# Optimization experiments

Hardware: AMD Instinct MI355X
Metric: run time of the kernel (lower is better)

The kernel has to match this reference:

```python
import jax, jax.numpy as jnp
import numpy as np

C = 64; H = 80; W = 120; B = 2; V = 3; BV = B * V; D = 20
NEAR = 0.1; FAR = 100.0
BF16 = jnp.bfloat16


def conv2d(x, w, b, pad):
    y = jax.lax.conv_general_dilated(x, w, (1, 1), [(pad, pad), (pad, pad)],
                                     dimension_numbers=('NCHW', 'OIHW', 'NCHW'))
    return y + b[None, :, None, None]


def bn2d(x, g, b, m, v, eps=1e-5):
    # BatchNorm2d in inference mode (running stats)
    scale = g / jnp.sqrt(v + eps)
    return (x - m[None, :, None, None]) * scale[None, :, None, None] + b[None, :, None, None]


def grid_sample(feat, grid):
    # feat [N,C,Hf,Wf], grid [N,Hg,Wg,2] in [-1,1]; bilinear, zeros padding, align_corners=True
    _, _, Hf, Wf = feat.shape
    gx = (grid[..., 0] + 1.0) * 0.5 * (Wf - 1)
    gy = (grid[..., 1] + 1.0) * 0.5 * (Hf - 1)
    x0 = jnp.floor(gx); y0 = jnp.floor(gy)

    def one(f, gx, gy, x0, y0):
        def gather(xi, yi):
            valid = (xi >= 0) & (xi < Wf) & (yi >= 0) & (yi < Hf)
            xc = jnp.clip(xi, 0, Wf - 1).astype(jnp.int32)
            yc = jnp.clip(yi, 0, Hf - 1).astype(jnp.int32)
            return f[:, yc, xc] * valid.astype(f.dtype)
        wx = gx - x0; wy = gy - y0
        return (gather(x0, y0) * ((1 - wx) * (1 - wy))
                + gather(x0 + 1, y0) * (wx * (1 - wy))
                + gather(x0, y0 + 1) * ((1 - wx) * wy)
                + gather(x0 + 1, y0 + 1) * (wx * wy))
    return jax.vmap(one)(feat, gx, gy, x0, y0)


def forward(x, intrinsics, c2ws,
            pf_bn1_g, pf_bn1_b, pf_bn1_m, pf_bn1_v, pf_w1, pf_b1,
            pf_bn2_g, pf_bn2_b, pf_bn2_m, pf_bn2_v, pf_w2, pf_b2,
            cp_w, cp_b, cf_bn_g, cf_bn_b, cf_bn_m, cf_bn_v, cf_w, cf_b):
    # ---- flag[0]: predicted depth -> world xyz, position_fusion ----
    depth = 255.0 * (0.5 * jnp.tanh(x[:, 0]) + 0.5)                       # [BV,H,W]
    d16 = depth.astype(BF16)
    ug = jnp.broadcast_to(jnp.arange(W, dtype=jnp.float32)[None, :], (H, W)).astype(BF16)
    vg = jnp.broadcast_to(jnp.arange(H, dtype=jnp.float32)[:, None], (H, W)).astype(BF16)
    cam = jnp.stack([ug[None] * d16, vg[None] * d16, d16], axis=-1).reshape(BV, H * W, 3)
    Kinv = jnp.linalg.inv(intrinsics.astype(jnp.float32)).astype(BF16)
    xyz = jnp.einsum('nij,npj->npi', Kinv, cam)                           # cam coords
    xyz = jnp.einsum('nij,npj->npi', c2ws[:, :3, :3].astype(BF16), xyz) \
          + c2ws[:, :3, 3].astype(BF16)[:, None, :]                       # world coords
    xyz = xyz.reshape(BV, H, W, 3).transpose(0, 3, 1, 2).astype(x.dtype)
    h = jnp.concatenate([xyz, x], axis=1)                                 # [BV,C+3,H,W]
    h = jax.nn.silu(conv2d(bn2d(h, pf_bn1_g, pf_bn1_b, pf_bn1_m, pf_bn1_v), pf_w1, pf_b1, 4))
    h = jax.nn.silu(conv2d(bn2d(h, pf_bn2_g, pf_bn2_b, pf_bn2_m, pf_bn2_v), pf_w2, pf_b2, 4))

    # ---- flag[1]: multi-view plane-sweep correlation ----
    xr = h.reshape(B, V, C, H, W)
    vb = lambda t: t.transpose(1, 0, 2, 3, 4).reshape(BV, C, H, W)        # 'b v ... -> (v b) ...'
    feat01 = vb(xr)
    Ki = intrinsics.reshape(B, V, 3, 3)
    intr_curr = jax.lax.stop_gradient(
        (Ki * jnp.array([W, H, 1.0], jnp.float32)[None, None, :, None]).transpose(1, 0, 2, 3).reshape(BV, 3, 3))
    E = jax.lax.stop_gradient(c2ws.reshape(B, V, 4, 4))
    Einv = jnp.linalg.inv(E)
    dmin, dmax = 1.0 / FAR, 1.0 / NEAR
    depth_vals = 1.0 / (dmin + jnp.linspace(0.0, 1.0, D) * (dmax - dmin))  # [D]
    pix = jnp.stack([jnp.broadcast_to(jnp.arange(W, dtype=jnp.float32)[None, :], (H, W)),
                     jnp.broadcast_to(jnp.arange(H, dtype=jnp.float32)[:, None], (H, W)),
                     jnp.ones((H, W), jnp.float32)], 0).reshape(3, H * W)
    Kinv_c = jnp.linalg.inv(intr_curr).astype(BF16)

    corr = 0.0
    for idx in range(1, V):
        order = list(range(V))[idx:] + list(range(V))[:idx]
        feat10 = vb(xr[:, jnp.array(order)])                              # [BV,C,H,W]
        pose = jnp.concatenate([E[:, o] @ Einv[:, v0] for v0, o in enumerate(order)], axis=0)  # [BV,4,4]
        pts = jnp.einsum('bij,jp->bip', Kinv_c, pix.astype(BF16))
        pts = jnp.einsum('bij,bjp->bip', pose[:, :3, :3].astype(BF16), pts)
        pts = pts[:, :, None, :] * depth_vals.astype(BF16)[None, None, :, None] \
              + pose[:, :3, 3].astype(BF16)[:, :, None, None]             # [BV,3,D,HW]
        pts = jnp.einsum('bij,bjdp->bidp', intr_curr.astype(BF16), pts).astype(jnp.float32)
        den = jnp.maximum(pts[:, 2], 1e-3)
        grid = jnp.stack([2.0 * pts[:, 0] / den / (W - 1) - 1.0,
                          2.0 * pts[:, 1] / den / (H - 1) - 1.0], axis=-1)
        grid = jax.lax.stop_gradient(grid.reshape(BV, D * H, W, 2))
        warped = grid_sample(feat10, grid).reshape(BV, C, D, H, W)
        corr = corr + jnp.einsum('bchw,bcdhw->bdhw', feat01, warped) / (C ** 0.5)
    corr = corr / (V - 1)

    cin = jnp.concatenate([corr, feat01], axis=1)                         # [BV,D+C,H,W]
    cost = conv2d(cin, cp_w, cp_b, 1).reshape(V, B, C, H, W).transpose(1, 0, 2, 3, 4)
    fused = jnp.concatenate([cost, xr], axis=2).reshape(BV, 2 * C, H, W)
    out = jax.nn.silu(conv2d(bn2d(fused, cf_bn_g, cf_bn_b, cf_bn_m, cf_bn_v), cf_w, cf_b, 4))
    return out


def setup_inputs() -> dict:
    key = jax.random.key(0)
    ks = jax.random.split(key, 24)
    def nrm(i, shape, scale=1.0):
        return scale * jax.random.normal(ks[i], shape, jnp.float32)
    def wconv(i, shape):
        fan_in = int(np.prod(shape[1:]))
        return jax.random.normal(ks[i], shape, jnp.float32) / np.sqrt(fan_in)
    x = nrm(0, (BV, C, H, W))
    Kmat = np.tile(np.array([[1.2, 0, 0.5], [0, 1.6, 0.5], [0, 0, 1.0]], np.float32), (BV, 1, 1))
    intrinsics = jnp.asarray(Kmat)
    c2_list = []
    for i in range(BV):
        th = 0.3 * (i % V) - 0.3
        T = np.eye(4, dtype=np.float32)
        T[:3, :3] = np.array([[np.cos(th), 0, np.sin(th)], [0, 1, 0], [-np.sin(th), 0, np.cos(th)]], np.float32)
        T[:3, 3] = [0.5 * (i % V) - 0.5, 0.0, 0.1]
        c2_list.append(T)
    c2ws = jnp.asarray(np.stack(c2_list))
    # first BN sees raw world-xyz channels (magnitude ~1e4), so realistic running var there
    bn1_v = jnp.concatenate([jnp.full((3,), 1e8, jnp.float32), jnp.ones((C,), jnp.float32)])
    return dict(
        x=x, intrinsics=intrinsics, c2ws=c2ws,
        pf_bn1_g=1.0 + 0.1 * nrm(1, (C + 3,)), pf_bn1_b=0.1 * nrm(2, (C + 3,)),
        pf_bn1_m=0.1 * nrm(3, (C + 3,)), pf_bn1_v=bn1_v,
        pf_w1=wconv(4, (C, C + 3, 9, 9)), pf_b1=0.01 * nrm(5, (C,)),
        pf_bn2_g=1.0 + 0.1 * nrm(6, (C,)), pf_bn2_b=0.1 * nrm(7, (C,)),
        pf_bn2_m=0.1 * nrm(8, (C,)), pf_bn2_v=jnp.ones((C,), jnp.float32),
        pf_w2=wconv(9, (C, C, 9, 9)), pf_b2=0.01 * nrm(10, (C,)),
        cp_w=wconv(11, (C, C + D, 3, 3)), cp_b=0.01 * nrm(12, (C,)),
        cf_bn_g=1.0 + 0.1 * nrm(13, (2 * C,)), cf_bn_b=0.1 * nrm(14, (2 * C,)),
        cf_bn_m=0.1 * nrm(15, (2 * C,)), cf_bn_v=jnp.ones((2 * C,), jnp.float32),
        cf_w=wconv(16, (C, 2 * C, 9, 9)), cf_b=0.01 * nrm(17, (C,)))


def reference(x, intrinsics, c2ws,
              pf_bn1_g, pf_bn1_b, pf_bn1_m, pf_bn1_v, pf_w1, pf_b1,
              pf_bn2_g, pf_bn2_b, pf_bn2_m, pf_bn2_v, pf_w2, pf_b2,
              cp_w, cp_b, cf_bn_g, cf_bn_b, cf_bn_m, cf_bn_v, cf_w, cf_b):
    return forward(x, intrinsics, c2ws,
                   pf_bn1_g, pf_bn1_b, pf_bn1_m, pf_bn1_v, pf_w1, pf_b1,
                   pf_bn2_g, pf_bn2_b, pf_bn2_m, pf_bn2_v, pf_w2, pf_b2,
                   cp_w, cp_b, cf_bn_g, cf_bn_b, cf_bn_m, cf_bn_v, cf_w, cf_b)
```

## Files before the change

### kernel.cpp

```cpp
#include <hip/hip_runtime.h>
#include <math.h>

static constexpr int kH  = 80;
static constexpr int kW  = 120;
static constexpr int kHW = kH * kW;
static constexpr int kBV = 6;
static constexpr int kD  = 20;

typedef __attribute__((ext_vector_type(8)))  short bf16x8;
typedef __attribute__((ext_vector_type(16))) float f32x16;
typedef __attribute__((ext_vector_type(4)))  int   i32x4;
typedef __attribute__((ext_vector_type(2)))  int   i32x2;
typedef __attribute__((ext_vector_type(4)))  float float4v;

__device__ __forceinline__ float bf16r(float x) {
  unsigned u = __float_as_uint(x);
  u += 0x7FFFu + ((u >> 16) & 1u);
  return __uint_as_float(u & 0xFFFF0000u);
}
__device__ __forceinline__ unsigned short bf16c(float x) {
  unsigned u = __float_as_uint(x);
  u += 0x7FFFu + ((u >> 16) & 1u);
  return (unsigned short)(u >> 16);
}
__device__ __forceinline__ int pack2(float a, float b) {
  return (int)((unsigned)bf16c(a) | ((unsigned)bf16c(b) << 16));
}

struct ConstBuf {
  float bn1_s[67], bn1_o[67];
  float bn2_s[64], bn2_o[64];
  float bnf_s[128], bnf_o[128];
  float Kinv[6][9];
  float Rw[6][9];
  float tw[6][3];
  float Kinvc[6][9];
  float intrc[6][9];
  float poseR[2][6][9];
  float poseT[2][6][3];
  float dvals[20];
};

__device__ void inv3x3(const float* A, float* o) {
  float a = A[0], b = A[1], c = A[2];
  float d = A[3], e = A[4], f = A[5];
  float g = A[6], h = A[7], i = A[8];
  float det = a * (e * i - f * h) - b * (d * i - f * g) + c * (d * h - e * g);
  float id = 1.0f / det;
  o[0] = (e * i - f * h) * id;
  o[1] = -(b * i - c * h) * id;
  o[2] = (b * f - c * e) * id;
  o[3] = -(d * i - f * g) * id;
  o[4] = (a * i - c * g) * id;
  o[5] = -(a * f - c * d) * id;
  o[6] = (d * h - e * g) * id;
  o[7] = -(a * h - b * g) * id;
  o[8] = (a * e - b * d) * id;
}

__device__ void inv4x4(const float* A, float* out) {
  float M[4][8];
  for (int r = 0; r < 4; ++r) {
    for (int c = 0; c < 4; ++c) M[r][c] = A[r * 4 + c];
    for (int c = 0; c < 4; ++c) M[r][4 + c] = (r == c) ? 1.0f : 0.0f;
  }
  for (int col = 0; col < 4; ++col) {
    int p = col;
    float best = fabsf(M[col][col]);
    for (int r = col + 1; r < 4; ++r) {
      float v = fabsf(M[r][col]);
      if (v > best) { best = v; p = r; }
    }
    if (p != col)
      for (int c = 0; c < 8; ++c) { float t = M[col][c]; M[col][c] = M[p][c]; M[p][c] = t; }
    float inv = 1.0f / M[col][col];
    for (int c = 0; c < 8; ++c) M[col][c] *= inv;
    for (int r = 0; r < 4; ++r) {
      if (r == col) continue;
      float f = M[r][col];
      for (int c = 0; c < 8; ++c) M[r][c] -= f * M[col][c];
    }
  }
  for (int r = 0; r < 4; ++r)
    for (int c = 0; c < 4; ++c) out[r * 4 + c] = M[r][4 + c];
}

__device__ void mm4(const float* A, const float* B, float* C) {
  for (int r = 0; r < 4; ++r)
    for (int c = 0; c < 4; ++c) {
      float s = 0.0f;
      for (int k = 0; k < 4; ++k) s += A[r * 4 + k] * B[k * 4 + c];
      C[r * 4 + c] = s;
    }
}

__global__ void consts_kernel(const float* __restrict__ intr, const float* __restrict__ c2,
                              const float* g1, const float* b1, const float* m1, const float* v1,
                              const float* g2, const float* b2, const float* m2, const float* v2,
                              const float* gf, const float* bff, const float* mf, const float* vff,
                              ConstBuf* cb) {
  int tid = threadIdx.x;
  for (int c = tid; c < 67; c += 64) {
    float s = g1[c] / sqrtf(v1[c] + 1e-5f);
    cb->bn1_s[c] = s; cb->bn1_o[c] = b1[c] - m1[c] * s;
  }
  for (int c = tid; c < 64; c += 64) {
    float s = g2[c] / sqrtf(v2[c] + 1e-5f);
    cb->bn2_s[c] = s; cb->bn2_o[c] = b2[c] - m2[c] * s;
  }
  for (int c = tid; c < 128; c += 64) {
    float s = gf[c] / sqrtf(vff[c] + 1e-5f);
    cb->bnf_s[c] = s; cb->bnf_o[c] = bff[c] - mf[c] * s;
  }
  if (tid < 20) {
    float l = (1.0f / 19.0f) * (float)tid;
    cb->dvals[tid] = bf16r(1.0f / (0.01f + l * 9.99f));
  }
  __shared__ float Einv_s[6][16];
  if (tid < 6) {
    float Ki[9];
    inv3x3(intr + tid * 9, Ki);
    for (int k = 0; k < 9; ++k) cb->Kinv[tid][k] = bf16r(Ki[k]);
    const float* T = c2 + tid * 16;
    cb->Rw[tid][0] = bf16r(T[0]);  cb->Rw[tid][1] = bf16r(T[1]);  cb->Rw[tid][2] = bf16r(T[2]);
    cb->Rw[tid][3] = bf16r(T[4]);  cb->Rw[tid][4] = bf16r(T[5]);  cb->Rw[tid][5] = bf16r(T[6]);
    cb->Rw[tid][6] = bf16r(T[8]);  cb->Rw[tid][7] = bf16r(T[9]);  cb->Rw[tid][8] = bf16r(T[10]);
    cb->tw[tid][0] = bf16r(T[3]);  cb->tw[tid][1] = bf16r(T[7]);  cb->tw[tid][2] = bf16r(T[11]);
    inv4x4(T, Einv_s[tid]);
    int vj = tid >> 1, bj = tid & 1, ii = bj * 3 + vj;
    const float* Kk = intr + ii * 9;
    float S[9] = {Kk[0] * 120.0f, Kk[1] * 120.0f, Kk[2] * 120.0f,
                  Kk[3] * 80.0f,  Kk[4] * 80.0f,  Kk[5] * 80.0f,
                  Kk[6],          Kk[7],          Kk[8]};
    for (int k = 0; k < 9; ++k) cb->intrc[tid][k] = bf16r(S[k]);
    float Si[9];
    inv3x3(S, Si);
    for (int k = 0; k < 9; ++k) cb->Kinvc[tid][k] = bf16r(Si[k]);
  }
  __syncthreads();
  if (tid < 12) {
    int t = tid / 6, jj = tid % 6;
    int vj = jj >> 1, bj = jj & 1;
    int o = (vj + t + 1) % 3;
    float P[16];
    mm4(c2 + (bj * 3 + o) * 16, Einv_s[bj * 3 + vj], P);
    for (int r = 0; r < 3; ++r) {
      for (int c = 0; c < 3; ++c) cb->poseR[t][jj][r * 3 + c] = bf16r(P[r * 4 + c]);
      cb->poseT[t][jj][r] = bf16r(P[r * 4 + 3]);
    }
  }
}

template <int K, int CINP, int CINR>
__global__ __launch_bounds__(256)
void prep_w(const float* __restrict__ w, unsigned short* __restrict__ Wp) {
  constexpr int NCH = CINP / 32;
  constexpr int NU = K * K * NCH * 256;
  int u = blockIdx.x * 256 + threadIdx.x;
  if (u >= NU) return;
  int slot = u & 255;
  int rest = u >> 8;
  int ci = rest % NCH;
  int kk = rest / NCH;
  int ky = kk / K, kx = kk - ky * K;
  int oc = slot >> 2;
  int gi = (slot & 3) ^ ((oc >> 2) & 3);
  int chb = ci * 32 + gi * 8;
  unsigned short o[8];
#pragma unroll
  for (int e = 0; e < 8; ++e) {
    int ch = chb + e;
    float val = (ch < CINR) ? w[(((size_t)oc * CINR + ch) * K + ky) * K + kx] : 0.0f;
    o[e] = bf16c(val);
  }
  i32x4 pk;
  pk.x = (int)o[0] | ((int)o[1] << 16);
  pk.y = (int)o[2] | ((int)o[3] << 16);
  pk.z = (int)o[4] | ((int)o[5] << 16);
  pk.w = (int)o[6] | ((int)o[7] << 16);
  *(i32x4*)&Wp[(size_t)u * 8] = pk;
}

__global__ __launch_bounds__(256)
void hn_pack(const float* __restrict__ x, const ConstBuf* __restrict__ cb,
             unsigned short* __restrict__ hn_b) {
  int id = blockIdx.x * 256 + threadIdx.x;
  if (id >= kBV * kHW) return;
  int bv = id / kHW, pix = id - bv * kHW;
  int yy = pix / kW, xx = pix - yy * kW;
  float t0 = tanhf(x[(size_t)bv * 64 * kHW + pix]);
  float depth = 255.0f * (0.5f * t0 + 0.5f);
  float dz = bf16r(depth);
  float cx = bf16r((float)xx * dz);
  float cy = bf16r((float)yy * dz);
  const float* Ki = cb->Kinv[bv];
  float p0 = bf16r(Ki[0] * cx + Ki[1] * cy + Ki[2] * dz);
  float p1 = bf16r(Ki[3] * cx + Ki[4] * cy + Ki[5] * dz);
  float p2 = bf16r(Ki[6] * cx + Ki[7] * cy + Ki[8] * dz);
  const float* R = cb->Rw[bv];
  const float* tw = cb->tw[bv];
  float q[3];
  q[0] = bf16r(bf16r(R[0] * p0 + R[1] * p1 + R[2] * p2) + tw[0]);
  q[1] = bf16r(bf16r(R[3] * p0 + R[4] * p1 + R[5] * p2) + tw[1]);
  q[2] = bf16r(bf16r(R[6] * p0 + R[7] * p1 + R[8] * p2) + tw[2]);
  unsigned short* o = &hn_b[(size_t)id * 96];
  const float* xb = x + (size_t)bv * 64 * kHW + pix;
#pragma unroll
  for (int g = 0; g < 24; ++g) {
    float vv[4];
#pragma unroll
    for (int e = 0; e < 4; ++e) {
      int ch = g * 4 + e;
      float val;
      if (ch < 3) val = q[ch] * cb->bn1_s[ch] + cb->bn1_o[ch];
      else if (ch < 67) val = xb[(size_t)(ch - 3) * kHW] * cb->bn1_s[ch] + cb->bn1_o[ch];
      else val = 0.0f;
      vv[e] = val;
    }
    i32x2 pk = {pack2(vv[0], vv[1]), pack2(vv[2], vv[3])};
    *(i32x2*)(o + g * 4) = pk;
  }
}

template <int CINP, int K, int OUT>
__global__ __launch_bounds__(256)
void conv_mfma(const unsigned short* __restrict__ in_b,
               const unsigned short* __restrict__ Wp,
               const float* __restrict__ bias,
               const ConstBuf* __restrict__ cb,
               float* __restrict__ outf,
               unsigned short* __restrict__ outb) {
  constexpr int NCH = CINP / 32;
  constexpr int KK = K * K;
  constexpr int GN = KK / 3;
  constexpr int PAD = K / 2;
  constexpr int NC = 16 + K - 1;
  constexpr int NR = 8 + K - 1;
  constexpr int NPX = NC * NR;
  __shared__ unsigned short sA[NPX * 32];
  __shared__ unsigned short sB[2][3 * 2048];

  const int tid = threadIdx.x;
  const int w = tid >> 6, l = tid & 63;
  const int bx = blockIdx.x, by = blockIdx.y, bz = blockIdx.z;
  const size_t inbase = (size_t)bz * kHW;

  const int r = l & 31, h = l >> 5;
  const int xloc = r & 15;
  const int ybase = 2 * w + (r >> 4);
  f32x16 acc[2] = {};

  int boff[2][2];
#pragma unroll
  for (int nt = 0; nt < 2; ++nt)
#pragma unroll
    for (int kc = 0; kc < 2; ++kc) {
      int oc = nt * 32 + (l & 31);
      int gi = kc * 2 + h;
      boff[nt][kc] = (oc * 4 + (gi ^ ((oc >> 2) & 3))) * 8;
    }

  for (int ci = 0; ci < NCH; ++ci) {
    for (int g2 = tid; g2 < NPX * 4; g2 += 256) {
      int px = g2 >> 2, gi = g2 & 3;
      int hy = px / NC, hx = px - hy * NC;
      int gy = by * 8 - PAD + hy, gx = bx * 16 - PAD + hx;
      bool ok = ((unsigned)gy < (unsigned)kH) && ((unsigned)gx < (unsigned)kW);
      i32x4 v = {0, 0, 0, 0};
      if (ok) v = *(const i32x4*)&in_b[(inbase + gy * kW + gx) * CINP + ci * 32 + gi * 8];
      *(i32x4*)&sA[px * 32 + ((gi ^ ((px >> 2) & 3)) << 3)] = v;
    }
#pragma unroll
    for (int t = 0; t < 3; ++t) {
      int u = tid + t * 256;
      int kki = u >> 8, slot = u & 255;
      *(i32x4*)&sB[0][u * 8] =
          *(const i32x4*)&Wp[(((size_t)kki * NCH + ci) * 256 + slot) * 8];
    }
    __syncthreads();

    for (int g = 0; g < GN; ++g) {
      const int cur = g & 1, nxt = cur ^ 1;
      const bool hasnext = (g + 1 < GN);
      i32x4 pf[3];
      if (hasnext) {
#pragma unroll
        for (int t = 0; t < 3; ++t) {
          int u = tid + t * 256;
          int kki = u >> 8, slot = u & 255;
          pf[t] = *(const i32x4*)
              &Wp[(((size_t)((g + 1) * 3 + kki) * NCH + ci) * 256 + slot) * 8];
        }
      }
#pragma unroll
      for (int kki = 0; kki < 3; ++kki) {
        const int kk = g * 3 + kki;
        const int ky = kk / K, kx = kk - ky * K;
        const int hp = (ybase + ky) * NC + (xloc + kx);
        bf16x8 a[2];
#pragma unroll
        for (int kc = 0; kc < 2; ++kc) {
          int gi = kc * 2 + h;
          a[kc] = *(const bf16x8*)&sA[hp * 32 + ((gi ^ ((hp >> 2) & 3)) << 3)];
        }
        bf16x8 bb[2][2];
#pragma unroll
        for (int nt = 0; nt < 2; ++nt)
#pragma unroll
          for (int kc = 0; kc < 2; ++kc)
            bb[nt][kc] = *(const bf16x8*)&sB[cur][kki * 2048 + boff[nt][kc]];
#pragma unroll
        for (int nt = 0; nt < 2; ++nt) {
          acc[nt] = __builtin_amdgcn_mfma_f32_32x32x16_bf16(a[0], bb[nt][0], acc[nt], 0, 0, 0);
          acc[nt] = __builtin_amdgcn_mfma_f32_32x32x16_bf16(a[1], bb[nt][1], acc[nt], 0, 0, 0);
        }
      }
      if (hasnext) {
#pragma unroll
        for (int t = 0; t < 3; ++t)
          *(i32x4*)&sB[nxt][(tid + t * 256) * 8] = pf[t];
      }
      __syncthreads();
    }
  }

#pragma unroll
  for (int nt = 0; nt < 2; ++nt) {
    const int oc = nt * 32 + (l & 31);
    const float bs = bias[oc];
    float s2 = 0.f, o2 = 0.f;
    if (OUT == 0) { s2 = cb->bn2_s[oc]; o2 = cb->bn2_o[oc]; }
    if (OUT == 2) { s2 = cb->bnf_s[oc]; o2 = cb->bnf_o[oc]; }
#pragma unroll
    for (int reg = 0; reg < 16; ++reg) {
      int row = (reg & 3) + 8 * (reg >> 2) + 4 * h;
      int x = bx * 16 + (row & 15);
      if (x >= kW) continue;
      int y = by * 8 + 2 * w + (row >> 4);
      float v = acc[nt][reg] + bs;
      if (OUT != 2) v = v / (1.0f + expf(-v));
      if (OUT == 0) {
        size_t px = inbase + y * kW + x;
        outb[px * 64 + oc] = bf16c(v * s2 + o2);
      } else if (OUT == 1) {
        size_t px = inbase + y * kW + x;
        outf[px * 64 + oc] = v;
      } else if (OUT == 2) {
        int i = (bz & 1) * 3 + (bz >> 1);
        size_t px = (size_t)i * kHW + y * kW + x;
        outb[px * 128 + oc] = bf16c(v * s2 + o2);
      } else {
        outf[((size_t)bz * 64 + oc) * kHW + y * kW + x] = v;
      }
    }
  }
}

__global__ __launch_bounds__(256)
void corr_kernel(const float* __restrict__ h, const ConstBuf* __restrict__ cb,
                 unsigned short* __restrict__ cin_b) {
  __shared__ float sgeo[4][40][8];
  const int tid = threadIdx.x;
  const int w = tid >> 6, lane = tid & 63;
  const int wid = blockIdx.x * 4 + w;
  const int j = wid / kHW;
  const int pix = wid - j * kHW;
  const int yy = pix / kW, xx = pix - yy * kW;
  const int b = j & 1, v = j >> 1;
  const float f01 = h[((size_t)(b * 3 + v) * kHW + pix) * 64 + lane];
  const char* sb0 = (const char*)(h + (size_t)(b * 3 + ((v + 1) % 3)) * kHW * 64);
  const char* sb1 = (const char*)(h + (size_t)(b * 3 + ((v + 2) % 3)) * kHW * 64);

  if (lane < 40) {
    const int d = lane >> 1, t = lane & 1;
    const float* Kc = cb->Kinvc[j];
    const float* IC = cb->intrc[j];
    const float uf = (float)xx, vf = (float)yy;
    float p1_0 = bf16r(Kc[0] * uf + Kc[1] * vf + Kc[2]);
    float p1_1 = bf16r(Kc[3] * uf + Kc[4] * vf + Kc[5]);
    float p1_2 = bf16r(Kc[6] * uf + Kc[7] * vf + Kc[8]);
    const float* PR = cb->poseR[t][j];
    const float* PT = cb->poseT[t][j];
    float p20 = bf16r(PR[0] * p1_0 + PR[1] * p1_1 + PR[2] * p1_2);
    float p21 = bf16r(PR[3] * p1_0 + PR[4] * p1_1 + PR[5] * p1_2);
    float p22 = bf16r(PR[6] * p1_0 + PR[7] * p1_1 + PR[8] * p1_2);
    float dv = cb->dvals[d];
    float q0 = bf16r(bf16r(p20 * dv) + PT[0]);
    float q1 = bf16r(bf16r(p21 * dv) + PT[1]);
    float q2 = bf16r(bf16r(p22 * dv) + PT[2]);
    float s0 = bf16r(IC[0] * q0 + IC[1] * q1 + IC[2] * q2);
    float s1 = bf16r(IC[3] * q0 + IC[4] * q1 + IC[5] * q2);
    float s2 = bf16r(IC[6] * q0 + IC[7] * q1 + IC[8] * q2);
    float den = fmaxf(s2, 1e-3f);
    float g0 = 2.0f * s0 / den / 119.0f - 1.0f;
    float g1 = 2.0f * s1 / den / 79.0f - 1.0f;
    float gx = (g0 + 1.0f) * 0.5f * 119.0f;
    float gy = (g1 + 1.0f) * 0.5f * 79.0f;
    float x0f = floorf(gx), y0f = floorf(gy);
    float wx = gx - x0f, wy = gy - y0f;
    float x1f = x0f + 1.0f, y1f = y0f + 1.0f;
    float vx0 = (x0f >= 0.0f && x0f < 120.0f) ? 1.0f : 0.0f;
    float vx1 = (x1f >= 0.0f && x1f < 120.0f) ? 1.0f : 0.0f;
    float vy0 = (y0f >= 0.0f && y0f < 80.0f) ? 1.0f : 0.0f;
    float vy1 = (y1f >= 0.0f && y1f < 80.0f) ? 1.0f : 0.0f;
    int xi0 = (int)fminf(fmaxf(x0f, 0.0f), 119.0f);
    int xi1 = (int)fminf(fmaxf(x1f, 0.0f), 119.0f);
    int yi0 = (int)fminf(fmaxf(y0f, 0.0f), 79.0f);
    int yi1 = (int)fminf(fmaxf(y1f, 0.0f), 79.0f);
    int r0b = yi0 * (kW * 256), r1b = yi1 * (kW * 256);
    int c0b = xi0 * 256, c1b = xi1 * 256;
    float* gp = sgeo[w][lane];
    gp[0] = __int_as_float(r0b + c0b);
    gp[1] = __int_as_float(r0b + c1b);
    gp[2] = __int_as_float(r1b + c0b);
    gp[3] = __int_as_float(r1b + c1b);
    gp[4] = ((1.0f - wx) * (1.0f - wy)) * (vx0 * vy0);
    gp[5] = (wx * (1.0f - wy)) * (vx1 * vy0);
    gp[6] = ((1.0f - wx) * wy) * (vx0 * vy1);
    gp[7] = (wx * wy) * (vx1 * vy1);
  }
  __syncthreads();

  const unsigned lane4 = (unsigned)lane * 4u;
  unsigned short* op = &cin_b[(size_t)wid * 96];
#pragma unroll 2
  for (int d = 0; d < kD; ++d) {
    float a = 0.0f;
#pragma unroll
    for (int t = 0; t < 2; ++t) {
      const char* sb = t ? sb1 : sb0;
      const float* gp = sgeo[w][d * 2 + t];
      float4v ga = *(const float4v*)gp;
      float4v gb = *(const float4v*)(gp + 4);
      float v00 = *(const float*)(sb + ((unsigned)__float_as_int(ga.x) + lane4));
      float v10 = *(const float*)(sb + ((unsigned)__float_as_int(ga.y) + lane4));
      float v01 = *(const float*)(sb + ((unsigned)__float_as_int(ga.z) + lane4));
      float v11 = *(const float*)(sb + ((unsigned)__float_as_int(ga.w) + lane4));
      a += gb.x * v00 + gb.y * v10 + gb.z * v01 + gb.w * v11;
    }
    float r = a * f01;
#pragma unroll
    for (int off = 32; off > 0; off >>= 1) r += __shfl_xor(r, off, 64);
    if (lane == 0) op[d] = bf16c(r * 0.0625f);
  }
}

__global__ __launch_bounds__(256)
void pack_cin(const float* __restrict__ h, unsigned short* __restrict__ cin_b) {
  int id = blockIdx.x * 256 + threadIdx.x;
  if (id >= kBV * kHW) return;
  int j = id / kHW, pix = id - j * kHW;
  int src = (j & 1) * 3 + (j >> 1);
  const float* hr = &h[((size_t)src * kHW + pix) * 64];
  unsigned short* o = &cin_b[(size_t)id * 96];
#pragma unroll
  for (int g = 0; g < 16; ++g) {
    float4v vv = *(const float4v*)(hr + g * 4);
    i32x2 pk = {pack2(vv.x, vv.y), pack2(vv.z, vv.w)};
    *(i32x2*)(o + 20 + g * 4) = pk;
  }
  i32x2 z = {0, 0};
  *(i32x2*)(o + 84) = z;
  *(i32x2*)(o + 88) = z;
  *(i32x2*)(o + 92) = z;
}

__global__ __launch_bounds__(256)
void pack_fusedn(const float* __restrict__ h, const ConstBuf* __restrict__ cb,
                 unsigned short* __restrict__ fusedn_b) {
  int id = blockIdx.x * 256 + threadIdx.x;
  if (id >= kBV * kHW) return;
  const float* hr = &h[(size_t)id * 64];
  unsigned short* o = &fusedn_b[(size_t)id * 128 + 64];
#pragma unroll
  for (int g = 0; g < 16; ++g) {
    float4v vv = *(const float4v*)(hr + g * 4);
    float r0 = vv.x * cb->bnf_s[64 + g * 4 + 0] + cb->bnf_o[64 + g * 4 + 0];
    float r1 = vv.y * cb->bnf_s[64 + g * 4 + 1] + cb->bnf_o[64 + g * 4 + 1];
    float r2 = vv.z * cb->bnf_s[64 + g * 4 + 2] + cb->bnf_o[64 + g * 4 + 2];
    float r3 = vv.w * cb->bnf_s[64 + g * 4 + 3] + cb->bnf_o[64 + g * 4 + 3];
    i32x2 pk = {pack2(r0, r1), pack2(r2, r3)};
    *(i32x2*)(o + g * 4) = pk;
  }
}

extern "C" void kernel_launch(void* const* d_in, const int* in_sizes, int n_in,
                              void* d_out, int out_size, void* d_ws, size_t ws_size,
                              hipStream_t stream) {
  (void)in_sizes; (void)n_in; (void)out_size; (void)ws_size;
  const float* x    = (const float*)d_in[0];
  const float* intr = (const float*)d_in[1];
  const float* c2w  = (const float*)d_in[2];
  const float* bn1g = (const float*)d_in[3];
  const float* bn1b = (const float*)d_in[4];
  const float* bn1m = (const float*)d_in[5];
  const float* bn1v = (const float*)d_in[6];
  const float* w1   = (const float*)d_in[7];
  const float* b1   = (const float*)d_in[8];
  const float* bn2g = (const float*)d_in[9];
  const float* bn2b = (const float*)d_in[10];
  const float* bn2m = (const float*)d_in[11];
  const float* bn2v = (const float*)d_in[12];
  const float* w2   = (const float*)d_in[13];
  const float* b2   = (const float*)d_in[14];
  const float* cpw  = (const float*)d_in[15];
  const float* cpb  = (const float*)d_in[16];
  const float* bnfg = (const float*)d_in[17];
  const float* bnfb = (const float*)d_in[18];
  const float* bnfm = (const float*)d_in[19];
  const float* bnfv = (const float*)d_in[20];
  const float* wf   = (const float*)d_in[21];
  const float* bff  = (const float*)d_in[22];

  char* ws = (char*)d_ws;
  ConstBuf* cb            = (ConstBuf*)ws;
  unsigned short* hn_b    = (unsigned short*)(ws + 8192);
  unsigned short* h1_b    = (unsigned short*)(ws + 11067392);
  float*          h       = (float*)(ws + 18440192);
  unsigned short* cin_b   = (unsigned short*)(ws + 33185792);
  unsigned short* fused_b = (unsigned short*)(ws + 44244992);
  unsigned short* Wp1     = (unsigned short*)(ws + 58990592);
  unsigned short* Wp2     = (unsigned short*)(ws + 59985920);
  unsigned short* Wpc     = (unsigned short*)(ws + 60649472);
  unsigned short* Wpf     = (unsigned short*)(ws + 60760064);

  consts_kernel<<<1, 64, 0, stream>>>(intr, c2w, bn1g, bn1b, bn1m, bn1v,
                                      bn2g, bn2b, bn2m, bn2v, bnfg, bnfb, bnfm, bnfv, cb);
  prep_w<9, 96, 67><<<243, 256, 0, stream>>>(w1, Wp1);
  prep_w<9, 64, 64><<<162, 256, 0, stream>>>(w2, Wp2);
  prep_w<3, 96, 84><<<27, 256, 0, stream>>>(cpw, Wpc);
  prep_w<9, 128, 128><<<324, 256, 0, stream>>>(wf, Wpf);
  hn_pack<<<225, 256, 0, stream>>>(x, cb, hn_b);

  dim3 cgrid(8, 10, 6);
  conv_mfma<96, 9, 0><<<cgrid, 256, 0, stream>>>(hn_b, Wp1, b1, cb, nullptr, h1_b);
  conv_mfma<64, 9, 1><<<cgrid, 256, 0, stream>>>(h1_b, Wp2, b2, cb, h, nullptr);
  corr_kernel<<<14400, 256, 0, stream>>>(h, cb, cin_b);
  pack_cin<<<225, 256, 0, stream>>>(h, cin_b);
  conv_mfma<96, 3, 2><<<cgrid, 256, 0, stream>>>(cin_b, Wpc, cpb, cb, nullptr, fused_b);
  pack_fusedn<<<225, 256, 0, stream>>>(h, cb, fused_b);
  conv_mfma<128, 9, 3><<<cgrid, 256, 0, stream>>>(fused_b, Wpf, bff, cb, (float*)d_out, nullptr);
}
```

Baseline: 403.0 us.

## Store conv2 output as bf16, fuse pack kernels into conv2 epilogue and corr

Conv2 now writes its output as bf16 and also writes the BN-normalized half of the fusion input directly, which removes the pack_fusedn kernel. The correlation kernel reads bf16 features with each wave handling two pixels (32 lanes each, two channels per lane). It also writes the feature copy and zero padding into cin, which removes pack_cin. The goal is to halve gather traffic and drop two launches. The cost is rounding the correlation features to bf16 earlier than before, which may change numerics slightly.

```diff
diff --git a/kernel.cpp b/kernel.cpp
--- a/kernel.cpp
+++ b/kernel.cpp
@@ -25,6 +25,12 @@
 }
 __device__ __forceinline__ int pack2(float a, float b) {
   return (int)((unsigned)bf16c(a) | ((unsigned)bf16c(b) << 16));
+}
+__device__ __forceinline__ float bl(unsigned pk) {
+  return __uint_as_float(pk << 16);
+}
+__device__ __forceinline__ float bh(unsigned pk) {
+  return __uint_as_float(pk & 0xFFFF0000u);
 }
 
 struct ConstBuf {
@@ -229,7 +235,8 @@
                const float* __restrict__ bias,
                const ConstBuf* __restrict__ cb,
                float* __restrict__ outf,
-               unsigned short* __restrict__ outb) {
+               unsigned short* __restrict__ outb,
+               unsigned short* __restrict__ outb2) {
   constexpr int NCH = CINP / 32;
   constexpr int KK = K * K;
   constexpr int GN = KK / 3;
@@ -330,6 +337,7 @@
     const float bs = bias[oc];
     float s2 = 0.f, o2 = 0.f;
     if (OUT == 0) { s2 = cb->bn2_s[oc]; o2 = cb->bn2_o[oc]; }
+    if (OUT == 1) { s2 = cb->bnf_s[64 + oc]; o2 = cb->bnf_o[64 + oc]; }
     if (OUT == 2) { s2 = cb->bnf_s[oc]; o2 = cb->bnf_o[oc]; }
 #pragma unroll
     for (int reg = 0; reg < 16; ++reg) {
@@ -344,7 +352,8 @@
         outb[px * 64 + oc] = bf16c(v * s2 + o2);
       } else if (OUT == 1) {
         size_t px = inbase + y * kW + x;
-        outf[px * 64 + oc] = v;
+        outb[px * 64 + oc] = bf16c(v);
+        outb2[px * 128 + 64 + oc] = bf16c(v * s2 + o2);
       } else if (OUT == 2) {
         int i = (bz & 1) * 3 + (bz >> 1);
         size_t px = (size_t)i * kHW + y * kW + x;
@@ -357,25 +366,32 @@
 }
 
 __global__ __launch_bounds__(256)
-void corr_kernel(const float* __restrict__ h, const ConstBuf* __restrict__ cb,
+void corr_kernel(const unsigned short* __restrict__ h_b, const ConstBuf* __restrict__ cb,
                  unsigned short* __restrict__ cin_b) {
-  __shared__ float sgeo[4][40][8];
+  __shared__ float sgeo[4][2][40][8];
   const int tid = threadIdx.x;
   const int w = tid >> 6, lane = tid & 63;
-  const int wid = blockIdx.x * 4 + w;
-  const int j = wid / kHW;
-  const int pix = wid - j * kHW;
-  const int yy = pix / kW, xx = pix - yy * kW;
+  const int pair = blockIdx.x * 4 + w;
+  const int j = pair / (kHW / 2);
+  const int pix = (pair - j * (kHW / 2)) * 2;
   const int b = j & 1, v = j >> 1;
-  const float f01 = h[((size_t)(b * 3 + v) * kHW + pix) * 64 + lane];
-  const char* sb0 = (const char*)(h + (size_t)(b * 3 + ((v + 1) % 3)) * kHW * 64);
-  const char* sb1 = (const char*)(h + (size_t)(b * 3 + ((v + 2) % 3)) * kHW * 64);
-
-  if (lane < 40) {
-    const int d = lane >> 1, t = lane & 1;
+  const int ph = lane >> 5, cl = lane & 31;
+  const int pixl = pix + ph;
+  const int dst = b * 3 + v;
+  const unsigned f01pk =
+      ((const unsigned*)(h_b + ((size_t)dst * kHW + pixl) * 64))[cl];
+  const float f01lo = bl(f01pk), f01hi = bh(f01pk);
+  const char* sb0 = (const char*)(h_b + (size_t)(b * 3 + ((v + 1) % 3)) * kHW * 64);
+  const char* sb1 = (const char*)(h_b + (size_t)(b * 3 + ((v + 2) % 3)) * kHW * 64);
+
+  for (int job = lane; job < 80; job += 64) {
+    const int p = job / 40, jj = job - p * 40;
+    const int d = jj >> 1, t = jj & 1;
+    const int pp = pix + p;
+    const int yyp = pp / kW, xxp = pp - yyp * kW;
     const float* Kc = cb->Kinvc[j];
     const float* IC = cb->intrc[j];
-    const float uf = (float)xx, vf = (float)yy;
+    const float uf = (float)xxp, vf = (float)yyp;
     float p1_0 = bf16r(Kc[0] * uf + Kc[1] * vf + Kc[2]);
     float p1_1 = bf16r(Kc[3] * uf + Kc[4] * vf + Kc[5]);
     float p1_2 = bf16r(Kc[6] * uf + Kc[7] * vf + Kc[8]);
@@ -407,9 +423,9 @@
     int xi1 = (int)fminf(fmaxf(x1f, 0.0f), 119.0f);
     int yi0 = (int)fminf(fmaxf(y0f, 0.0f), 79.0f);
     int yi1 = (int)fminf(fmaxf(y1f, 0.0f), 79.0f);
-    int r0b = yi0 * (kW * 256), r1b = yi1 * (kW * 256);
-    int c0b = xi0 * 256, c1b = xi1 * 256;
-    float* gp = sgeo[w][lane];
+    int r0b = yi0 * (kW * 128), r1b = yi1 * (kW * 128);
+    int c0b = xi0 * 128, c1b = xi1 * 128;
+    float* gp = sgeo[w][p][jj];
     gp[0] = __int_as_float(r0b + c0b);
     gp[1] = __int_as_float(r0b + c1b);
     gp[2] = __int_as_float(r1b + c0b);
@@ -421,66 +437,31 @@
   }
   __syncthreads();
 
-  const unsigned lane4 = (unsigned)lane * 4u;
-  unsigned short* op = &cin_b[(size_t)wid * 96];
+  unsigned short* op = &cin_b[(size_t)(j * kHW + pixl) * 96];
+  *(unsigned*)(op + 20 + 2 * cl) = f01pk;
+  if (cl < 6) *(unsigned*)(op + 84 + 2 * cl) = 0u;
+
+  const unsigned cl4 = (unsigned)cl * 4u;
 #pragma unroll 2
   for (int d = 0; d < kD; ++d) {
     float a = 0.0f;
 #pragma unroll
     for (int t = 0; t < 2; ++t) {
       const char* sb = t ? sb1 : sb0;
-      const float* gp = sgeo[w][d * 2 + t];
+      const float* gp = sgeo[w][ph][d * 2 + t];
       float4v ga = *(const float4v*)gp;
       float4v gb = *(const float4v*)(gp + 4);
-      float v00 = *(const float*)(sb + ((unsigned)__float_as_int(ga.x) + lane4));
-      float v10 = *(const float*)(sb + ((unsigned)__float_as_int(ga.y) + lane4));
-      float v01 = *(const float*)(sb + ((unsigned)__float_as_int(ga.z) + lane4));
-      float v11 = *(const float*)(sb + ((unsigned)__float_as_int(ga.w) + lane4));
-      a += gb.x * v00 + gb.y * v10 + gb.z * v01 + gb.w * v11;
-    }
-    float r = a * f01;
-#pragma unroll
-    for (int off = 32; off > 0; off >>= 1) r += __shfl_xor(r, off, 64);
-    if (lane == 0) op[d] = bf16c(r * 0.0625f);
-  }
-}
-
-__global__ __launch_bounds__(256)
-void pack_cin(const float* __restrict__ h, unsigned short* __restrict__ cin_b) {
-  int id = blockIdx.x * 256 + threadIdx.x;
-  if (id >= kBV * kHW) return;
-  int j = id / kHW, pix = id - j * kHW;
-  int src = (j & 1) * 3 + (j >> 1);
-  const float* hr = &h[((size_t)src * kHW + pix) * 64];
-  unsigned short* o = &cin_b[(size_t)id * 96];
-#pragma unroll
-  for (int g = 0; g < 16; ++g) {
-    float4v vv = *(const float4v*)(hr + g * 4);
-    i32x2 pk = {pack2(vv.x, vv.y), pack2(vv.z, vv.w)};
-    *(i32x2*)(o + 20 + g * 4) = pk;
-  }
-  i32x2 z = {0, 0};
-  *(i32x2*)(o + 84) = z;
-  *(i32x2*)(o + 88) = z;
-  *(i32x2*)(o + 92) = z;
-}
-
-__global__ __launch_bounds__(256)
-void pack_fusedn(const float* __restrict__ h, const ConstBuf* __restrict__ cb,
-                 unsigned short* __restrict__ fusedn_b) {
-  int id = blockIdx.x * 256 + threadIdx.x;
-  if (id >= kBV * kHW) return;
-  const float* hr = &h[(size_t)id * 64];
-  unsigned short* o = &fusedn_b[(size_t)id * 128 + 64];
-#pragma unroll
-  for (int g = 0; g < 16; ++g) {
-    float4v vv = *(const float4v*)(hr + g * 4);
-    float r0 = vv.x * cb->bnf_s[64 + g * 4 + 0] + cb->bnf_o[64 + g * 4 + 0];
-    float r1 = vv.y * cb->bnf_s[64 + g * 4 + 1] + cb->bnf_o[64 + g * 4 + 1];
-    float r2 = vv.z * cb->bnf_s[64 + g * 4 + 2] + cb->bnf_o[64 + g * 4 + 2];
-    float r3 = vv.w * cb->bnf_s[64 + g * 4 + 3] + cb->bnf_o[64 + g * 4 + 3];
-    i32x2 pk = {pack2(r0, r1), pack2(r2, r3)};
-    *(i32x2*)(o + g * 4) = pk;
+      unsigned k00 = *(const unsigned*)(sb + ((unsigned)__float_as_int(ga.x) + cl4));
+      unsigned k10 = *(const unsigned*)(sb + ((unsigned)__float_as_int(ga.y) + cl4));
+      unsigned k01 = *(const unsigned*)(sb + ((unsigned)__float_as_int(ga.z) + cl4));
+      unsigned k11 = *(const unsigned*)(sb + ((unsigned)__float_as_int(ga.w) + cl4));
+      float al = gb.x * bl(k00) + gb.y * bl(k10) + gb.z * bl(k01) + gb.w * bl(k11);
+      float ah = gb.x * bh(k00) + gb.y * bh(k10) + gb.z * bh(k01) + gb.w * bh(k11);
+      a += al * f01lo + ah * f01hi;
+    }
+#pragma unroll
+    for (int off = 16; off > 0; off >>= 1) a += __shfl_xor(a, off, 64);
+    if (cl == 0) op[d] = bf16c(a * 0.0625f);
   }
 }
 
@@ -516,7 +497,7 @@
   ConstBuf* cb            = (ConstBuf*)ws;
   unsigned short* hn_b    = (unsigned short*)(ws + 8192);
   unsigned short* h1_b    = (unsigned short*)(ws + 11067392);
-  float*          h       = (float*)(ws + 18440192);
+  unsigned short* h_b     = (unsigned short*)(ws + 18440192);
   unsigned short* cin_b   = (unsigned short*)(ws + 33185792);
   unsigned short* fused_b = (unsigned short*)(ws + 44244992);
   unsigned short* Wp1     = (unsigned short*)(ws + 58990592);
@@ -533,11 +514,9 @@
   hn_pack<<<225, 256, 0, stream>>>(x, cb, hn_b);
 
   dim3 cgrid(8, 10, 6);
-  conv_mfma<96, 9, 0><<<cgrid, 256, 0, stream>>>(hn_b, Wp1, b1, cb, nullptr, h1_b);
-  conv_mfma<64, 9, 1><<<cgrid, 256, 0, stream>>>(h1_b, Wp2, b2, cb, h, nullptr);
-  corr_kernel<<<14400, 256, 0, stream>>>(h, cb, cin_b);
-  pack_cin<<<225, 256, 0, stream>>>(h, cin_b);
-  conv_mfma<96, 3, 2><<<cgrid, 256, 0, stream>>>(cin_b, Wpc, cpb, cb, nullptr, fused_b);
-  pack_fusedn<<<225, 256, 0, stream>>>(h, cb, fused_b);
-  conv_mfma<128, 9, 3><<<cgrid, 256, 0, stream>>>(fused_b, Wpf, bff, cb, (float*)d_out, nullptr);
-}
+  conv_mfma<96, 9, 0><<<cgrid, 256, 0, stream>>>(hn_b, Wp1, b1, cb, nullptr, h1_b, nullptr);
+  conv_mfma<64, 9, 1><<<cgrid, 256, 0, stream>>>(h1_b, Wp2, b2, cb, nullptr, h_b, fused_b);
+  corr_kernel<<<7200, 256, 0, stream>>>(h_b, cb, cin_b);
+  conv_mfma<96, 3, 2><<<cgrid, 256, 0, stream>>>(cin_b, Wpc, cpb, cb, nullptr, fused_b, nullptr);
+  conv_mfma<128, 9, 3><<<cgrid, 256, 0, stream>>>(fused_b, Wpf, bff, cb, (float*)d_out, nullptr, nullptr);
+}
```

After: 340.6 us. 1.18x faster.
